# Optimization experiments

Measured on AMD Instinct MI355X. Metric: run time of the kernel, lower is better.

Reference implementation:

```python
import jax, jax.numpy as jnp
import numpy as np

HEAD_SIZE = 128
BLOCK_SIZE = 2048


def setup_inputs() -> dict:
    key = jax.random.key(0)
    kx, kk, kq, kv = jax.random.split(key, 4)
    B, T, C = 8, 2048, HEAD_SIZE
    s = 1.0 / np.sqrt(C)
    x = jax.random.normal(kx, (B, T, C), dtype=jnp.float32)
    Wk = jax.random.normal(kk, (C, C), dtype=jnp.float32) * s
    Wq = jax.random.normal(kq, (C, C), dtype=jnp.float32) * s
    Wv = jax.random.normal(kv, (C, C), dtype=jnp.float32) * s
    return {"x": x, "Wk": Wk, "Wq": Wq, "Wv": Wv}


def reference(x, Wk, Wq, Wv):
    B, T, C = x.shape
    # nn.Linear(C, C, bias=False): y = x @ W.T
    k = jnp.einsum('btc,dc->btd', x, Wk)
    q = jnp.einsum('btc,dc->btd', x, Wq)
    v = jnp.einsum('btc,dc->btd', x, Wv)
    scores = jnp.einsum('btd,bsd->bts', q, k) * (C ** -0.5)  # [B,T,T]
    causal = jnp.tril(jnp.ones((T, T), dtype=bool))
    scores = jnp.where(causal, scores, -jnp.inf)
    weights = jax.nn.softmax(scores, axis=-1)
    return jnp.einsum('bts,bsd->btd', weights, v)
```

## Files before the change

kernel.cpp:

```cpp
#include <hip/hip_runtime.h>

#define T_SEQ 2048
#define C_DIM 128
#define S_QK 0.08838834764831845f

typedef __attribute__((ext_vector_type(8))) short bf16x8;
typedef __attribute__((ext_vector_type(4))) float f32x4;

#define OPART_OFF 12582912UL
#define ML_OFF    31457280UL
#define XBF_OFF   31752192UL
#define WBF_OFF   35946496UL

__device__ __forceinline__ unsigned short f2bf(float f) {
    union { float f; unsigned int u; } v; v.f = f;
    unsigned int r = v.u + 0x7FFFu + ((v.u >> 16) & 1u);
    return (unsigned short)(r >> 16);
}

__device__ __forceinline__ int chunk_base(int qt) {
    int g = qt >> 3;
    if (g == 1) return (qt - 8) * 2;
    if (g == 2) return 16 + (qt - 16) * 3;
    return 40 + (qt - 24) * 4;
}

__global__ __launch_bounds__(256) void prep_kernel(
    const float* __restrict__ x,
    const float* __restrict__ Wk, const float* __restrict__ Wq,
    const float* __restrict__ Wv,
    unsigned short* __restrict__ xbf, unsigned short* __restrict__ wbf)
{
    int idx = blockIdx.x * 256 + threadIdx.x;
    const float* src;
    unsigned short* dst;
    float scale = 1.0f;
    if (idx < 524288) {
        src = x + (size_t)idx * 4;
        dst = xbf + (size_t)idx * 4;
    } else {
        int wi  = idx - 524288;
        int sel = wi >> 12;
        int off = (wi & 4095) * 4;
        src = (sel == 0 ? Wq : sel == 1 ? Wk : Wv) + off;
        dst = wbf + sel * 16384 + off;
        if (sel == 0) scale = S_QK;
    }
    float4 v = *reinterpret_cast<const float4*>(src);
    ushort4 o;
    o.x = f2bf(v.x * scale); o.y = f2bf(v.y * scale);
    o.z = f2bf(v.z * scale); o.w = f2bf(v.w * scale);
    *reinterpret_cast<ushort4*>(dst) = o;
}

__global__ __launch_bounds__(256) void proj_kernel(
    const unsigned short* __restrict__ xbf,
    const unsigned short* __restrict__ wbf,
    unsigned short* __restrict__ qo, unsigned short* __restrict__ ko,
    unsigned short* __restrict__ vto)
{
    const int rt = blockIdx.x;
    const int z  = blockIdx.y;
    const int tid  = threadIdx.x;
    const int lane = tid & 63;
    const int w    = tid >> 6;
    const int n16  = lane & 15;
    const int quad = lane >> 4;

    __shared__ __align__(16) unsigned short Wl[128 * 136];
    __shared__ __align__(16) unsigned short Xl[9216];

    const unsigned short* Wsrc = wbf + z * 16384;
    #pragma unroll
    for (int i = 0; i < 8; ++i) {
        int e = (tid + i * 256) * 8;
        int r = e >> 7, c = e & 127;
        *reinterpret_cast<uint4*>(&Wl[r * 136 + c]) =
            *reinterpret_cast<const uint4*>(Wsrc + e);
    }
    const unsigned short* xrow = xbf + (size_t)rt * 64 * C_DIM;
    #pragma unroll
    for (int i = 0; i < 4; ++i) {
        int e = (tid + i * 256) * 8;
        int r = e >> 7, c = e & 127;
        *reinterpret_cast<uint4*>(&Xl[r * 136 + c]) =
            *reinterpret_cast<const uint4*>(xrow + e);
    }
    __syncthreads();

    const int arow = w * 16 + n16;
    bf16x8 afr[4];
    #pragma unroll
    for (int kk = 0; kk < 4; ++kk)
        afr[kk] = *reinterpret_cast<const bf16x8*>(&Xl[arow * 136 + kk * 32 + quad * 8]);

    f32x4 acc[8];
    #pragma unroll
    for (int nt = 0; nt < 8; ++nt) acc[nt] = (f32x4){0.f, 0.f, 0.f, 0.f};
    #pragma unroll
    for (int kk = 0; kk < 4; ++kk)
        #pragma unroll
        for (int nt = 0; nt < 8; ++nt) {
            bf16x8 bfr = *reinterpret_cast<const bf16x8*>(
                &Wl[(nt * 16 + n16) * 136 + kk * 32 + quad * 8]);
            acc[nt] = __builtin_amdgcn_mfma_f32_16x16x32_bf16(afr[kk], bfr, acc[nt], 0, 0, 0);
        }

    const int trow_base = w * 16 + quad * 4;
    __syncthreads();
    if (z < 2) {
        #pragma unroll
        for (int nt = 0; nt < 8; ++nt)
            #pragma unroll
            for (int r = 0; r < 4; ++r)
                Xl[(trow_base + r) * 136 + nt * 16 + n16] = f2bf(acc[nt][r]);
        __syncthreads();
        unsigned short* dst = (z == 0 ? qo : ko) + (size_t)rt * 64 * C_DIM;
        #pragma unroll
        for (int i = 0; i < 4; ++i) {
            int e = (tid + i * 256) * 8;
            int r = e >> 7, c = e & 127;
            *reinterpret_cast<uint4*>(dst + e) =
                *reinterpret_cast<const uint4*>(&Xl[r * 136 + c]);
        }
    } else {
        const int b  = rt >> 5;
        const int qt = rt & 31;
        #pragma unroll
        for (int nt = 0; nt < 8; ++nt)
            #pragma unroll
            for (int r = 0; r < 4; ++r)
                Xl[(nt * 16 + n16) * 72 + trow_base + r] = f2bf(acc[nt][r]);
        __syncthreads();
        unsigned short* dst = vto + (size_t)b * C_DIM * T_SEQ + (size_t)qt * 64;
        #pragma unroll
        for (int i = 0; i < 4; ++i) {
            int e = tid + i * 256;
            int d = e >> 3, cv = (e & 7) * 8;
            *reinterpret_cast<uint4*>(dst + (size_t)d * T_SEQ + cv) =
                *reinterpret_cast<const uint4*>(&Xl[d * 72 + cv]);
        }
    }
}

__global__ __launch_bounds__(256) void attn_kernel(
    const unsigned short* __restrict__ qb,
    const unsigned short* __restrict__ kb,
    const unsigned short* __restrict__ vtb,
    float* __restrict__ opart, float2* __restrict__ mlbuf,
    float* __restrict__ out)
{
    const int qt    = blockIdx.x;
    const int chunk = blockIdx.y;
    const int b     = blockIdx.z;
    if (chunk * 8 > qt) return;

    const int tid  = threadIdx.x;
    const int lane = tid & 63;
    const int w    = tid >> 6;
    const int n16  = lane & 15;
    const int quad = lane >> 4;

    __shared__ __align__(16) unsigned short Kl[64 * 136];
    __shared__ __align__(16) unsigned short Vl[128 * 72];
    __shared__ __align__(16) unsigned short Pl[4][16 * 72];

    const size_t bT = (size_t)b * T_SEQ;
    const int qbase = qt * 64 + w * 16;

    bf16x8 qfr[4];
    #pragma unroll
    for (int kk = 0; kk < 4; ++kk)
        qfr[kk] = *reinterpret_cast<const bf16x8*>(
            qb + (bT + qbase + n16) * C_DIM + kk * 32 + quad * 8);

    f32x4 o[8];
    #pragma unroll
    for (int ct = 0; ct < 8; ++ct) o[ct] = (f32x4){0.f, 0.f, 0.f, 0.f};
    float m[4], l[4];
    #pragma unroll
    for (int r = 0; r < 4; ++r) { m[r] = -INFINITY; l[r] = 0.f; }

    const int k0 = chunk * 8;
    const int k1 = min(k0 + 8, qt + 1);

    for (int kt = k0; kt < k1; ++kt) {
        __syncthreads();
        const unsigned short* ks = kb + (bT + (size_t)kt * 64) * C_DIM;
        #pragma unroll
        for (int i = 0; i < 4; ++i) {
            int e = tid + i * 256;
            int r = e >> 4, c = (e & 15) * 8;
            *reinterpret_cast<uint4*>(&Kl[r * 136 + c]) =
                *reinterpret_cast<const uint4*>(ks + r * 128 + c);
        }
        const unsigned short* vs = vtb + (size_t)b * C_DIM * T_SEQ + (size_t)kt * 64;
        #pragma unroll
        for (int i = 0; i < 4; ++i) {
            int e = tid + i * 256;
            int d = e >> 3, c = (e & 7) * 8;
            *reinterpret_cast<uint4*>(&Vl[d * 72 + c]) =
                *reinterpret_cast<const uint4*>(vs + (size_t)d * T_SEQ + c);
        }
        __syncthreads();

        f32x4 s[4];
        #pragma unroll
        for (int nt = 0; nt < 4; ++nt) s[nt] = (f32x4){0.f, 0.f, 0.f, 0.f};
        #pragma unroll
        for (int kk = 0; kk < 4; ++kk)
            #pragma unroll
            for (int nt = 0; nt < 4; ++nt) {
                bf16x8 bfr = *reinterpret_cast<const bf16x8*>(
                    &Kl[(nt * 16 + n16) * 136 + kk * 32 + quad * 8]);
                s[nt] = __builtin_amdgcn_mfma_f32_16x16x32_bf16(qfr[kk], bfr, s[nt], 0, 0, 0);
            }

        if (kt == qt) {
            #pragma unroll
            for (int nt = 0; nt < 4; ++nt)
                #pragma unroll
                for (int r = 0; r < 4; ++r) {
                    int sabs = kt * 64 + nt * 16 + n16;
                    int qabs = qbase + quad * 4 + r;
                    if (sabs > qabs) s[nt][r] = -1e30f;
                }
        }

        float alpha[4];
        #pragma unroll
        for (int r = 0; r < 4; ++r) {
            float tmax = fmaxf(fmaxf(s[0][r], s[1][r]), fmaxf(s[2][r], s[3][r]));
            #pragma unroll
            for (int off = 1; off < 16; off <<= 1)
                tmax = fmaxf(tmax, __shfl_xor(tmax, off));
            float mn = fmaxf(m[r], tmax);
            alpha[r] = __expf(m[r] - mn);
            float tsum = 0.f;
            #pragma unroll
            for (int nt = 0; nt < 4; ++nt) {
                float p = __expf(s[nt][r] - mn);
                s[nt][r] = p;
                tsum += p;
            }
            #pragma unroll
            for (int off = 1; off < 16; off <<= 1)
                tsum += __shfl_xor(tsum, off);
            l[r] = l[r] * alpha[r] + tsum;
            m[r] = mn;
        }
        #pragma unroll
        for (int ct = 0; ct < 8; ++ct)
            #pragma unroll
            for (int r = 0; r < 4; ++r)
                o[ct][r] *= alpha[r];

        unsigned short* pw = Pl[w];
        #pragma unroll
        for (int nt = 0; nt < 4; ++nt)
            #pragma unroll
            for (int r = 0; r < 4; ++r)
                pw[(quad * 4 + r) * 72 + nt * 16 + n16] = f2bf(s[nt][r]);

        #pragma unroll
        for (int kk2 = 0; kk2 < 2; ++kk2) {
            bf16x8 afr = *reinterpret_cast<const bf16x8*>(
                &pw[n16 * 72 + kk2 * 32 + quad * 8]);
            #pragma unroll
            for (int ct = 0; ct < 8; ++ct) {
                bf16x8 bfr = *reinterpret_cast<const bf16x8*>(
                    &Vl[(ct * 16 + n16) * 72 + kk2 * 32 + quad * 8]);
                o[ct] = __builtin_amdgcn_mfma_f32_16x16x32_bf16(afr, bfr, o[ct], 0, 0, 0);
            }
        }
    }

    if (qt < 8) {
        float* outp = out + (bT + qbase) * C_DIM;
        #pragma unroll
        for (int r = 0; r < 4; ++r) {
            float inv = 1.0f / l[r];
            #pragma unroll
            for (int ct = 0; ct < 8; ++ct)
                outp[(size_t)(quad * 4 + r) * C_DIM + ct * 16 + n16] = o[ct][r] * inv;
        }
    } else {
        const int slot = b * 72 + chunk_base(qt) + chunk;
        float* op = opart + (size_t)slot * 8192;
        #pragma unroll
        for (int r = 0; r < 4; ++r) {
            int row = w * 16 + quad * 4 + r;
            #pragma unroll
            for (int ct = 0; ct < 8; ++ct)
                op[row * 128 + ct * 16 + n16] = o[ct][r];
            if (n16 == 0)
                mlbuf[(size_t)slot * 64 + row] = make_float2(m[r], l[r]);
        }
    }
}

__global__ __launch_bounds__(256) void merge_kernel(
    const float* __restrict__ opart, const float2* __restrict__ mlbuf,
    float* __restrict__ out)
{
    const int qt = 8 + blockIdx.x;
    const int b  = blockIdx.y;
    const int nch  = (qt >> 3) + 1;
    const int base = b * 72 + chunk_base(qt);
    const int row = threadIdx.x >> 2;
    const int c0  = (threadIdx.x & 3) * 32;

    float mi[4], li[4], wgt[4];
    float M = -INFINITY;
    for (int i = 0; i < nch; ++i) {
        float2 t = mlbuf[(size_t)(base + i) * 64 + row];
        mi[i] = t.x; li[i] = t.y;
        M = fmaxf(M, t.x);
    }
    float L = 0.f;
    for (int i = 0; i < nch; ++i) {
        wgt[i] = __expf(mi[i] - M);
        L += li[i] * wgt[i];
    }
    const float inv = 1.0f / L;

    float* orow = out + ((size_t)(b * T_SEQ + qt * 64 + row)) * C_DIM;
    #pragma unroll
    for (int j = 0; j < 8; ++j) {
        int col = c0 + j * 4;
        float ax = 0.f, ay = 0.f, az = 0.f, aw = 0.f;
        for (int i = 0; i < nch; ++i) {
            float4 p = *reinterpret_cast<const float4*>(
                opart + (size_t)(base + i) * 8192 + row * 128 + col);
            ax += wgt[i] * p.x; ay += wgt[i] * p.y;
            az += wgt[i] * p.z; aw += wgt[i] * p.w;
        }
        float4 r4; r4.x = ax * inv; r4.y = ay * inv; r4.z = az * inv; r4.w = aw * inv;
        *reinterpret_cast<float4*>(orow + col) = r4;
    }
}

extern "C" void kernel_launch(void* const* d_in, const int* in_sizes, int n_in,
                              void* d_out, int out_size, void* d_ws, size_t ws_size,
                              hipStream_t stream) {
    const float* x  = (const float*)d_in[0];
    const float* Wk = (const float*)d_in[1];
    const float* Wq = (const float*)d_in[2];
    const float* Wv = (const float*)d_in[3];

    unsigned short* qw  = (unsigned short*)d_ws;
    unsigned short* kw  = qw + 2097152;
    unsigned short* vw  = kw + 2097152;
    float*          opart = (float*)((char*)d_ws + OPART_OFF);
    float2*         mlb   = (float2*)((char*)d_ws + ML_OFF);
    unsigned short* xbf   = (unsigned short*)((char*)d_ws + XBF_OFF);
    unsigned short* wbf   = (unsigned short*)((char*)d_ws + WBF_OFF);

    prep_kernel<<<2096, 256, 0, stream>>>(x, Wk, Wq, Wv, xbf, wbf);
    proj_kernel<<<dim3(256, 3), 256, 0, stream>>>(xbf, wbf, qw, kw, vw);
    attn_kernel<<<dim3(32, 4, 8), 256, 0, stream>>>(qw, kw, vw, opart, mlb, (float*)d_out);
    merge_kernel<<<dim3(24, 8), 256, 0, stream>>>(opart, mlb, (float*)d_out);
}
```

Measured before the change: 135.5 us.

## Fuse bf16 conversion into projection and double-buffer attention K/V tiles via direct LDS loads

Removes the separate prep kernel: the projection kernel now reads fp32 x and weights directly and converts to bf16 in registers before writing to shared memory. The attention kernel stages K and V tiles with global_load_lds into XOR-swizzled, double-buffered shared memory, prefetching the next tile while computing the current one, with explicit waitcnt and barriers. The grid is linearized so that batch is the fastest-varying index. The projection kernel now re-reads and re-converts the fp32 weights in every block, and the hand-written waitcnt counts must stay consistent with the number of issued loads.

```diff
diff --git a/kernel.cpp b/kernel.cpp
--- a/kernel.cpp
+++ b/kernel.cpp
@@ -9,8 +9,11 @@
 
 #define OPART_OFF 12582912UL
 #define ML_OFF    31457280UL
-#define XBF_OFF   31752192UL
-#define WBF_OFF   35946496UL
+
+#define GLOAD_LDS16(gp, lp)                                          \
+    __builtin_amdgcn_global_load_lds(                                \
+        (const __attribute__((address_space(1))) void*)(gp),         \
+        (__attribute__((address_space(3))) void*)(lp), 16, 0, 0)
 
 __device__ __forceinline__ unsigned short f2bf(float f) {
     union { float f; unsigned int u; } v; v.f = f;
@@ -25,37 +28,10 @@
     return 40 + (qt - 24) * 4;
 }
 
-__global__ __launch_bounds__(256) void prep_kernel(
+__global__ __launch_bounds__(256) void proj_kernel(
     const float* __restrict__ x,
     const float* __restrict__ Wk, const float* __restrict__ Wq,
     const float* __restrict__ Wv,
-    unsigned short* __restrict__ xbf, unsigned short* __restrict__ wbf)
-{
-    int idx = blockIdx.x * 256 + threadIdx.x;
-    const float* src;
-    unsigned short* dst;
-    float scale = 1.0f;
-    if (idx < 524288) {
-        src = x + (size_t)idx * 4;
-        dst = xbf + (size_t)idx * 4;
-    } else {
-        int wi  = idx - 524288;
-        int sel = wi >> 12;
-        int off = (wi & 4095) * 4;
-        src = (sel == 0 ? Wq : sel == 1 ? Wk : Wv) + off;
-        dst = wbf + sel * 16384 + off;
-        if (sel == 0) scale = S_QK;
-    }
-    float4 v = *reinterpret_cast<const float4*>(src);
-    ushort4 o;
-    o.x = f2bf(v.x * scale); o.y = f2bf(v.y * scale);
-    o.z = f2bf(v.z * scale); o.w = f2bf(v.w * scale);
-    *reinterpret_cast<ushort4*>(dst) = o;
-}
-
-__global__ __launch_bounds__(256) void proj_kernel(
-    const unsigned short* __restrict__ xbf,
-    const unsigned short* __restrict__ wbf,
     unsigned short* __restrict__ qo, unsigned short* __restrict__ ko,
     unsigned short* __restrict__ vto)
 {
@@ -70,21 +46,28 @@
     __shared__ __align__(16) unsigned short Wl[128 * 136];
     __shared__ __align__(16) unsigned short Xl[9216];
 
-    const unsigned short* Wsrc = wbf + z * 16384;
+    const float* Wsrc = (z == 0 ? Wq : z == 1 ? Wk : Wv);
+    const float wscale = (z == 0) ? S_QK : 1.0f;
+    #pragma unroll
+    for (int i = 0; i < 16; ++i) {
+        int e = (tid + i * 256) * 4;
+        int r = e >> 7, c = e & 127;
+        float4 v = *reinterpret_cast<const float4*>(Wsrc + e);
+        ushort4 o4;
+        o4.x = f2bf(v.x * wscale); o4.y = f2bf(v.y * wscale);
+        o4.z = f2bf(v.z * wscale); o4.w = f2bf(v.w * wscale);
+        *reinterpret_cast<ushort4*>(&Wl[r * 136 + c]) = o4;
+    }
+    const float* xrow = x + (size_t)rt * 64 * C_DIM;
     #pragma unroll
     for (int i = 0; i < 8; ++i) {
-        int e = (tid + i * 256) * 8;
+        int e = (tid + i * 256) * 4;
         int r = e >> 7, c = e & 127;
-        *reinterpret_cast<uint4*>(&Wl[r * 136 + c]) =
-            *reinterpret_cast<const uint4*>(Wsrc + e);
-    }
-    const unsigned short* xrow = xbf + (size_t)rt * 64 * C_DIM;
-    #pragma unroll
-    for (int i = 0; i < 4; ++i) {
-        int e = (tid + i * 256) * 8;
-        int r = e >> 7, c = e & 127;
-        *reinterpret_cast<uint4*>(&Xl[r * 136 + c]) =
-            *reinterpret_cast<const uint4*>(xrow + e);
+        float4 v = *reinterpret_cast<const float4*>(xrow + e);
+        ushort4 o4;
+        o4.x = f2bf(v.x); o4.y = f2bf(v.y);
+        o4.z = f2bf(v.z); o4.w = f2bf(v.w);
+        *reinterpret_cast<ushort4*>(&Xl[r * 136 + c]) = o4;
     }
     __syncthreads();
 
@@ -140,6 +123,26 @@
             *reinterpret_cast<uint4*>(dst + (size_t)d * T_SEQ + cv) =
                 *reinterpret_cast<const uint4*>(&Xl[d * 72 + cv]);
         }
+    }
+}
+
+__device__ __forceinline__ void stage_tile(
+    const char* ksb, const char* vsb,
+    unsigned short* klbuf, unsigned short* vlbuf, int tid, int w)
+{
+    #pragma unroll
+    for (int it = 0; it < 4; ++it) {
+        const int L = it * 256 + tid;
+        const int r = L >> 4, c = L & 15;
+        GLOAD_LDS16(ksb + r * 256 + ((c ^ (r & 7)) << 4),
+                    klbuf + (size_t)(it * 256 + w * 64) * 8);
+    }
+    #pragma unroll
+    for (int it = 0; it < 4; ++it) {
+        const int L = it * 256 + tid;
+        const int r = L >> 3, c = L & 7;
+        GLOAD_LDS16(vsb + (size_t)r * (T_SEQ * 2) + ((c ^ (r & 7)) << 4),
+                    vlbuf + (size_t)(it * 256 + w * 64) * 8);
     }
 }
 
@@ -150,9 +153,11 @@
     float* __restrict__ opart, float2* __restrict__ mlbuf,
     float* __restrict__ out)
 {
-    const int qt    = blockIdx.x;
-    const int chunk = blockIdx.y;
-    const int b     = blockIdx.z;
+    const int lin   = blockIdx.x;
+    const int b     = lin & 7;
+    const int rest  = lin >> 3;
+    const int qt    = rest & 31;
+    const int chunk = rest >> 5;
     if (chunk * 8 > qt) return;
 
     const int tid  = threadIdx.x;
@@ -161,12 +166,20 @@
     const int n16  = lane & 15;
     const int quad = lane >> 4;
 
-    __shared__ __align__(16) unsigned short Kl[64 * 136];
-    __shared__ __align__(16) unsigned short Vl[128 * 72];
+    __shared__ __align__(16) unsigned short Kl[2][64 * 128];
+    __shared__ __align__(16) unsigned short Vl[2][128 * 64];
     __shared__ __align__(16) unsigned short Pl[4][16 * 72];
 
     const size_t bT = (size_t)b * T_SEQ;
     const int qbase = qt * 64 + w * 16;
+    const int k0 = chunk * 8;
+    const int k1 = min(k0 + 8, qt + 1);
+
+    const char* kbase = (const char*)(kb + bT * C_DIM);
+    const char* vbase = (const char*)(vtb + (size_t)b * C_DIM * T_SEQ);
+
+    stage_tile(kbase + (size_t)k0 * 64 * 256, vbase + (size_t)k0 * 128,
+               Kl[0], Vl[0], tid, w);
 
     bf16x8 qfr[4];
     #pragma unroll
@@ -181,28 +194,20 @@
     #pragma unroll
     for (int r = 0; r < 4; ++r) { m[r] = -INFINITY; l[r] = 0.f; }
 
-    const int k0 = chunk * 8;
-    const int k1 = min(k0 + 8, qt + 1);
-
-    for (int kt = k0; kt < k1; ++kt) {
-        __syncthreads();
-        const unsigned short* ks = kb + (bT + (size_t)kt * 64) * C_DIM;
-        #pragma unroll
-        for (int i = 0; i < 4; ++i) {
-            int e = tid + i * 256;
-            int r = e >> 4, c = (e & 15) * 8;
-            *reinterpret_cast<uint4*>(&Kl[r * 136 + c]) =
-                *reinterpret_cast<const uint4*>(ks + r * 128 + c);
-        }
-        const unsigned short* vs = vtb + (size_t)b * C_DIM * T_SEQ + (size_t)kt * 64;
-        #pragma unroll
-        for (int i = 0; i < 4; ++i) {
-            int e = tid + i * 256;
-            int d = e >> 3, c = (e & 7) * 8;
-            *reinterpret_cast<uint4*>(&Vl[d * 72 + c]) =
-                *reinterpret_cast<const uint4*>(vs + (size_t)d * T_SEQ + c);
-        }
-        __syncthreads();
+    int cur = 0;
+    for (int kt = k0; kt < k1; ++kt, cur ^= 1) {
+        if (kt + 1 < k1) {
+            stage_tile(kbase + (size_t)(kt + 1) * 64 * 256,
+                       vbase + (size_t)(kt + 1) * 128,
+                       Kl[cur ^ 1], Vl[cur ^ 1], tid, w);
+            asm volatile("s_waitcnt vmcnt(8)" ::: "memory");
+        } else {
+            asm volatile("s_waitcnt vmcnt(0)" ::: "memory");
+        }
+        __builtin_amdgcn_s_barrier();
+
+        const unsigned short* klc = Kl[cur];
+        const unsigned short* vlc = Vl[cur];
 
         f32x4 s[4];
         #pragma unroll
@@ -211,8 +216,9 @@
         for (int kk = 0; kk < 4; ++kk)
             #pragma unroll
             for (int nt = 0; nt < 4; ++nt) {
-                bf16x8 bfr = *reinterpret_cast<const bf16x8*>(
-                    &Kl[(nt * 16 + n16) * 136 + kk * 32 + quad * 8]);
+                const int rr = nt * 16 + n16;
+                const int p  = (kk * 4 + quad) ^ (n16 & 7);
+                bf16x8 bfr = *reinterpret_cast<const bf16x8*>(&klc[rr * 128 + p * 8]);
                 s[nt] = __builtin_amdgcn_mfma_f32_16x16x32_bf16(qfr[kk], bfr, s[nt], 0, 0, 0);
             }
 
@@ -268,11 +274,15 @@
                 &pw[n16 * 72 + kk2 * 32 + quad * 8]);
             #pragma unroll
             for (int ct = 0; ct < 8; ++ct) {
-                bf16x8 bfr = *reinterpret_cast<const bf16x8*>(
-                    &Vl[(ct * 16 + n16) * 72 + kk2 * 32 + quad * 8]);
+                const int rv = ct * 16 + n16;
+                const int p  = (kk2 * 4 + quad) ^ (n16 & 7);
+                bf16x8 bfr = *reinterpret_cast<const bf16x8*>(&vlc[rv * 64 + p * 8]);
                 o[ct] = __builtin_amdgcn_mfma_f32_16x16x32_bf16(afr, bfr, o[ct], 0, 0, 0);
             }
         }
+
+        asm volatile("s_waitcnt lgkmcnt(0)" ::: "memory");
+        __builtin_amdgcn_s_barrier();
     }
 
     if (qt < 8) {
@@ -353,11 +363,8 @@
     unsigned short* vw  = kw + 2097152;
     float*          opart = (float*)((char*)d_ws + OPART_OFF);
     float2*         mlb   = (float2*)((char*)d_ws + ML_OFF);
-    unsigned short* xbf   = (unsigned short*)((char*)d_ws + XBF_OFF);
-    unsigned short* wbf   = (unsigned short*)((char*)d_ws + WBF_OFF);
-
-    prep_kernel<<<2096, 256, 0, stream>>>(x, Wk, Wq, Wv, xbf, wbf);
-    proj_kernel<<<dim3(256, 3), 256, 0, stream>>>(xbf, wbf, qw, kw, vw);
-    attn_kernel<<<dim3(32, 4, 8), 256, 0, stream>>>(qw, kw, vw, opart, mlb, (float*)d_out);
+
+    proj_kernel<<<dim3(256, 3), 256, 0, stream>>>(x, Wk, Wq, Wv, qw, kw, vw);
+    attn_kernel<<<dim3(1024), 256, 0, stream>>>(qw, kw, vw, opart, mlb, (float*)d_out);
     merge_kernel<<<dim3(24, 8), 256, 0, stream>>>(opart, mlb, (float*)d_out);
 }
```

After: 125.1 us. -7.7%, faster.
